# Optimization experiments

Measured on AMD Instinct MI355X. Metric: run time of the kernel, lower is better.

Reference implementation:

```python
import jax, jax.numpy as jnp
import numpy as np

DIM = 64
HID = 32  # dim * 1/2
P = 4     # patch_size

def _conv1x1(x, w):
    # x: [B,C,H,W], w: [O,C] -> [B,O,H,W]
    return jnp.einsum('oc,bchw->bohw', w, x)

def _dwconv3x3(x, w):
    # depthwise 3x3, padding 1. x: [B,C,H,W], w: [C,1,3,3]
    return jax.lax.conv_general_dilated(
        x, w, window_strides=(1, 1), padding=((1, 1), (1, 1)),
        dimension_numbers=('NCHW', 'OIHW', 'NCHW'),
        feature_group_count=x.shape[1])

def setup_inputs() -> dict:
    key = jax.random.key(0)
    k1, k2, k3, k4 = jax.random.split(key, 4)
    B, H, W = 4, 512, 512
    x = jax.random.normal(k1, (B, DIM, H, W), dtype=jnp.float32)
    w_in1 = jax.random.normal(k2, (2 * HID, DIM), dtype=jnp.float32) * 0.05
    w_dw = jax.random.normal(k3, (2 * HID, 1, 3, 3), dtype=jnp.float32) * 0.1
    w_in2 = jax.random.normal(k4, (DIM, HID), dtype=jnp.float32) * 0.05
    w_freq = jnp.ones((DIM, 1, 1, P, P // 2 + 1), dtype=jnp.float32)
    return {'x': x, 'w_in1': w_in1, 'w_dw': w_dw, 'w_in2': w_in2, 'w_freq': w_freq}

def reference(x, w_in1, w_dw, w_in2, w_freq):
    shortcut = x
    y = _dwconv3x3(_conv1x1(x, w_in1), w_dw)          # [B,2*HID,H,W]
    y1, y2 = jnp.split(y, 2, axis=1)
    y = jax.nn.gelu(y1, approximate=False) * y2       # [B,HID,H,W]
    y = _conv1x1(y, w_in2)                            # [B,DIM,H,W]
    b, c, h, w = y.shape
    h_n = (P - h % P) % P
    w_n = (P - w % P) % P
    if h_n or w_n:
        y = jnp.pad(y, ((0, 0), (0, 0), (0, h_n), (0, w_n)), mode='reflect')
    hp, wp = y.shape[2] // P, y.shape[3] // P
    # [B,C,hp,P,wp,P] -> [B,C,hp,wp,P,P]
    yp = y.reshape(b, c, hp, P, wp, P).transpose(0, 1, 2, 4, 3, 5)
    yf = jnp.fft.rfft2(yp)                            # [B,C,hp,wp,P,P//2+1] complex
    yf = w_freq * yf                                  # w_freq broadcasts over (C,1,1,P,P//2+1)
    yp = jnp.fft.irfft2(yf, s=(P, P))
    y = yp.transpose(0, 1, 2, 4, 3, 5).reshape(b, c, hp * P, wp * P)
    y = y[:, :, :h, :w]
    return y + shortcut
```

## Files before the change

### kernel.cpp

```cpp
#include <hip/hip_runtime.h>
#include <hip/hip_fp16.h>
#include <math.h>

#define DIMC 64
#define HIDC 32
#define IMH 512
#define IMW 512
#define TW 32
#define TH 16
#define HW 34
#define HH 18
#define NPIX (HW*HH)
#define NPIXP 624
#define NCHUNK 39
#define VSTR 20
#define PLANE (IMH*IMW)

#define IDOFF 0
#define W1OFF 16
#define W2OFF 2064
#define PWOFF 3088

typedef _Float16 half8  __attribute__((ext_vector_type(8)));
typedef __fp16   fp16x2 __attribute__((ext_vector_type(2)));
typedef float f32x4     __attribute__((ext_vector_type(4)));
typedef unsigned int uint;

union U4H8 { uint4 u; half8 h; };

static __device__ __forceinline__ uint pkrtz(float a, float b) {
    union { fp16x2 h; uint u; } x;
    x.h = __builtin_amdgcn_cvt_pkrtz(a, b);
    return x.u;
}
static __device__ __forceinline__ float lo16f(uint u) {
    union { uint u; _Float16 h[2]; } x; x.u = u; return (float)x.h[0];
}
static __device__ __forceinline__ float hi16f(uint u) {
    union { uint u; _Float16 h[2]; } x; x.u = u; return (float)x.h[1];
}
static __device__ __forceinline__ uint pkfma(uint w, uint t, uint acc) {
    union { uint u; __half2 h; } W, T, A;
    W.u = w; T.u = t; A.u = acc;
    A.h = __hfma2(W.h, T.h, A.h);
    return A.u;
}

static __device__ __forceinline__ float gelu_f(float u) {
    const float z  = fabsf(u) * 0.70710678118654752f;
    const float t  = __builtin_amdgcn_rcpf(fmaf(0.3275911f, z, 1.0f));
    const float e  = __builtin_amdgcn_exp2f(-z * z * 1.4426950408889634f);
    float p = fmaf(t, 1.061405429f, -1.453152027f);
    p = fmaf(t, p, 1.421413741f);
    p = fmaf(t, p, -0.284496736f);
    p = fmaf(t, p, 0.254829592f);
    p = p * t;
    const float erf_abs = fmaf(-p, e, 1.0f);
    const float erfv = copysignf(erf_abs, u);
    return 0.5f * u * (1.0f + erfv);
}

__global__ __launch_bounds__(256)
void ffn_prep(const float* __restrict__ w1, const float* __restrict__ wdw,
              const float* __restrict__ w2, const float* __restrict__ wf,
              uint* __restrict__ ws)
{
    __shared__ int sid;
    const int tid = threadIdx.x;
    if (tid == 0) sid = 1;
    __syncthreads();
    bool ok = true;
    for (int i = tid; i < DIMC * 12; i += 256) ok = ok && (wf[i] == 1.0f);
    if (!ok) atomicAnd(&sid, 0);
    for (int i = tid; i < 2048; i += 256) ws[W1OFF + i] = pkrtz(w1[2*i], w1[2*i+1]);
    for (int i = tid; i < 1024; i += 256) ws[W2OFF + i] = pkrtz(w2[2*i], w2[2*i+1]);
    for (int i = tid; i < 288; i += 256) {
        const int k = i >> 5, ch = i & 31;
        ws[PWOFF + i] = pkrtz(wdw[ch*9 + k], wdw[(ch + HIDC)*9 + k]);
    }
    __syncthreads();
    if (tid == 0) ws[IDOFF] = (uint)sid;
}

__global__ __launch_bounds__(512, 4)
void ffn_main(const float* __restrict__ x,
              const uint*  __restrict__ ws,
              const float* __restrict__ wf,
              float* __restrict__ out)
{
    __shared__ uint ts[NPIXP * 32];

    const int tid = threadIdx.x;
    const int bid = ((blockIdx.x & 7) << 8) + (blockIdx.x >> 3);
    const int b  = bid >> 9;
    const int tr = bid & 511;
    const int ty = tr >> 4, tx = tr & 15;
    const int oy = ty * TH, ox = tx * TW;

    const float* xb = x + (size_t)b * DIMC * PLANE;

    {
        auto quad = [&](int T) {
            const int cg = T / 144;
            const int rm = T - cg * 144;
            const int r  = rm >> 3;
            const int q  = rm & 7;
            const int gy = oy + r - 1;
            const int p0 = r * HW + 1 + 4 * q;
            if ((unsigned)gy >= IMH) {
                #pragma unroll
                for (int j = 0; j < 4; ++j) {
                    const uint p = (uint)(p0 + j), base = p << 5, sw = (p & 7) << 2;
                    uint4 z = {0u, 0u, 0u, 0u};
                    *reinterpret_cast<uint4*>(&ts[base + (((uint)(cg*8))   ^ sw)]) = z;
                    *reinterpret_cast<uint4*>(&ts[base + (((uint)(cg*8+4)) ^ sw)]) = z;
                }
            } else {
                const float* xp = xb + (size_t)(cg*16) * PLANE + (size_t)gy * IMW + (ox + 4*q);
                f32x4 f[16];
                #pragma unroll
                for (int i = 0; i < 16; ++i)
                    f[i] = *reinterpret_cast<const f32x4*>(xp + (size_t)i * PLANE);
                #pragma unroll
                for (int j = 0; j < 4; ++j) {
                    const uint p = (uint)(p0 + j), base = p << 5, sw = (p & 7) << 2;
                    uint4 o0, o1;
                    o0.x = pkrtz(f[0][j],  f[1][j]);  o0.y = pkrtz(f[2][j],  f[3][j]);
                    o0.z = pkrtz(f[4][j],  f[5][j]);  o0.w = pkrtz(f[6][j],  f[7][j]);
                    o1.x = pkrtz(f[8][j],  f[9][j]);  o1.y = pkrtz(f[10][j], f[11][j]);
                    o1.z = pkrtz(f[12][j], f[13][j]); o1.w = pkrtz(f[14][j], f[15][j]);
                    *reinterpret_cast<uint4*>(&ts[base + (((uint)(cg*8))   ^ sw)]) = o0;
                    *reinterpret_cast<uint4*>(&ts[base + (((uint)(cg*8+4)) ^ sw)]) = o1;
                }
            }
        };
        auto edge = [&](int E) {
            const int cg = E / 36;
            const int rm = E - cg * 36;
            const int s  = rm / 18;
            const int r  = rm - s * 18;
            const int gy = oy + r - 1;
            const int gx = s ? (ox + TW) : (ox - 1);
            const uint p = (uint)(r * HW + (s ? 33 : 0));
            const uint base = p << 5, sw = (p & 7) << 2;
            if ((unsigned)gy >= IMH || (unsigned)gx >= IMW) {
                uint4 z = {0u, 0u, 0u, 0u};
                *reinterpret_cast<uint4*>(&ts[base + (((uint)(cg*8))   ^ sw)]) = z;
                *reinterpret_cast<uint4*>(&ts[base + (((uint)(cg*8+4)) ^ sw)]) = z;
            } else {
                const float* xp = xb + (size_t)(cg*16) * PLANE + (size_t)gy * IMW + gx;
                float f[16];
                #pragma unroll
                for (int i = 0; i < 16; ++i) f[i] = xp[(size_t)i * PLANE];
                uint4 o0, o1;
                o0.x = pkrtz(f[0], f[1]);   o0.y = pkrtz(f[2], f[3]);
                o0.z = pkrtz(f[4], f[5]);   o0.w = pkrtz(f[6], f[7]);
                o1.x = pkrtz(f[8], f[9]);   o1.y = pkrtz(f[10], f[11]);
                o1.z = pkrtz(f[12], f[13]); o1.w = pkrtz(f[14], f[15]);
                *reinterpret_cast<uint4*>(&ts[base + (((uint)(cg*8))   ^ sw)]) = o0;
                *reinterpret_cast<uint4*>(&ts[base + (((uint)(cg*8+4)) ^ sw)]) = o1;
            }
        };
        quad(tid);
        if (tid < 64) quad(512 + tid);
        if (tid >= 368) edge(tid - 368);
        if (tid < 12) {
            const uint p = (uint)(612 + tid);
            const uint base = p << 5, sw = (p & 7) << 2;
            uint4 z = {0u, 0u, 0u, 0u};
            #pragma unroll
            for (int g = 0; g < 8; ++g)
                *reinterpret_cast<uint4*>(&ts[base + (((uint)(g << 2)) ^ sw)]) = z;
        }
    }

    const int lane = tid & 63, wid = tid >> 6;
    const int l15 = lane & 15, lg = lane >> 4;
    const int li = tid >> 5, lj = tid & 31;

    half8 afrag1[4][2];
    const uint4* w1v = reinterpret_cast<const uint4*>(ws + W1OFF);
    #pragma unroll
    for (int mt = 0; mt < 4; ++mt)
        #pragma unroll
        for (int ks = 0; ks < 2; ++ks) {
            U4H8 u; u.u = w1v[(mt*16 + l15)*8 + ks*4 + lg];
            afrag1[mt][ks] = u.h;
        }
    half8 afrag2[4];
    const uint4* w2v = reinterpret_cast<const uint4*>(ws + W2OFF);
    #pragma unroll
    for (int mt = 0; mt < 4; ++mt) { U4H8 u; u.u = w2v[(mt*16 + l15)*4 + lg]; afrag2[mt] = u.h; }

    const uint ident = ws[IDOFF];
    __syncthreads();

    uint xs[4][4][2];
    #pragma unroll
    for (int cc = 0; cc < 4; ++cc) {
        const int px = wid*64 + cc*16 + l15;
        const int h  = ((px >> 5) + 1) * HW + (px & 31) + 1;
        const uint base = (uint)h << 5, sw = ((uint)h & 7) << 2;
        #pragma unroll
        for (int mt = 0; mt < 4; ++mt) {
            const uint a = base + (((uint)(mt*8 + lg*2)) ^ sw);
            xs[cc][mt][0] = ts[a];
            xs[cc][mt][1] = ts[a + 1];
        }
    }
    __syncthreads();

    for (int chunk = wid; chunk < NCHUNK; chunk += 8) {
        const uint px = (uint)(chunk*16 + l15);
        const uint base = px << 5, sw = (px & 7) << 2;
        f32x4 acc[4];
        #pragma unroll
        for (int mt = 0; mt < 4; ++mt) acc[mt] = (f32x4)0.0f;
        #pragma unroll
        for (int ks = 0; ks < 2; ++ks) {
            U4H8 u; u.u = *reinterpret_cast<const uint4*>(&ts[base + (((uint)(ks*16 + lg*4)) ^ sw)]);
            #pragma unroll
            for (int mt = 0; mt < 4; ++mt)
                acc[mt] = __builtin_amdgcn_mfma_f32_16x16x32_f16(afrag1[mt][ks], u.h, acc[mt], 0, 0, 0);
        }
        #pragma unroll
        for (int mt = 0; mt < 2; ++mt) {
            uint4 o;
            o.x = pkrtz(acc[mt][0], acc[mt+2][0]);
            o.y = pkrtz(acc[mt][1], acc[mt+2][1]);
            o.z = pkrtz(acc[mt][2], acc[mt+2][2]);
            o.w = pkrtz(acc[mt][3], acc[mt+2][3]);
            *reinterpret_cast<uint4*>(&ts[base + (((uint)(mt*16 + lg*4)) ^ sw)]) = o;
        }
    }
    __syncthreads();

    uint acc2[32];
    #pragma unroll
    for (int c = 0; c < 32; ++c) acc2[c] = 0u;
    #pragma unroll
    for (int k = 0; k < 9; ++k) {
        const int di = k / 3, dj = k - di * 3;
        const uint hpx = (uint)((li + di) * HW + (lj + dj));
        const uint base = hpx << 5, sw = (hpx & 7) << 2;
        const uint4* pwv = reinterpret_cast<const uint4*>(ws + PWOFF + k*32);
        #pragma unroll
        for (int g = 0; g < 8; ++g) {
            const uint4 wv = pwv[g];
            const uint4 tv = *reinterpret_cast<const uint4*>(&ts[base + (((uint)(g << 2)) ^ sw)]);
            acc2[g*4+0] = pkfma(wv.x, tv.x, acc2[g*4+0]);
            acc2[g*4+1] = pkfma(wv.y, tv.y, acc2[g*4+1]);
            acc2[g*4+2] = pkfma(wv.z, tv.z, acc2[g*4+2]);
            acc2[g*4+3] = pkfma(wv.w, tv.w, acc2[g*4+3]);
        }
    }
    uint4 vo[4];
    #pragma unroll
    for (int gg = 0; gg < 4; ++gg) {
        uint o[4];
        #pragma unroll
        for (int q = 0; q < 4; ++q) {
            const int c2 = gg*4 + q;
            const uint wa = acc2[2*c2], wb = acc2[2*c2 + 1];
            const float v0 = gelu_f(lo16f(wa)) * hi16f(wa);
            const float v1 = gelu_f(lo16f(wb)) * hi16f(wb);
            o[q] = pkrtz(v0, v1);
        }
        vo[gg].x = o[0]; vo[gg].y = o[1]; vo[gg].z = o[2]; vo[gg].w = o[3];
    }
    __syncthreads();
    {
        const uint vb = (uint)tid * VSTR;
        #pragma unroll
        for (int gg = 0; gg < 4; ++gg)
            *reinterpret_cast<uint4*>(&ts[vb + (uint)(gg << 2)]) = vo[gg];
    }
    __syncthreads();

    float* ob = out + (size_t)b * DIMC * PLANE;
    if (ident) {
        #pragma unroll
        for (int cc = 0; cc < 4; ++cc) {
            const uint px = (uint)(wid*64 + cc*16 + l15);
            U4H8 u; u.u = *reinterpret_cast<const uint4*>(&ts[px * VSTR + (uint)(lg << 2)]);
            const size_t pix = (size_t)(oy + (int)(px >> 5)) * IMW + (ox + (int)(px & 31));
            float* op = ob + pix;
            #pragma unroll
            for (int mt = 0; mt < 4; ++mt) {
                f32x4 a = __builtin_amdgcn_mfma_f32_16x16x32_f16(afrag2[mt], u.h, (f32x4)0.0f, 0, 0, 0);
                #pragma unroll
                for (int r = 0; r < 4; ++r) {
                    const int ch = mt*16 + lg*4 + r;
                    const uint xw = xs[cc][mt][r >> 1];
                    const float xv = (r & 1) ? hi16f(xw) : lo16f(xw);
                    op[(size_t)ch * PLANE] = a[r] + xv;
                }
            }
        }
    } else {
        float* ys = reinterpret_cast<float*>(ts + 10240);
        for (int mt = 0; mt < 4; ++mt) {
            __syncthreads();
            #pragma unroll
            for (int cc = 0; cc < 4; ++cc) {
                const uint px = (uint)(wid*64 + cc*16 + l15);
                U4H8 u; u.u = *reinterpret_cast<const uint4*>(&ts[px * VSTR + (uint)(lg << 2)]);
                f32x4 a = __builtin_amdgcn_mfma_f32_16x16x32_f16(afrag2[mt], u.h, (f32x4)0.0f, 0, 0, 0);
                #pragma unroll
                for (int r = 0; r < 4; ++r)
                    ys[(lg*4 + r) * 520 + (int)px] = a[r];
            }
            __syncthreads();
            {
                const int chl = tid >> 5;
                const int ch  = mt*16 + chl;
                const int pt  = tid & 31;
                const int pi = (pt >> 3) * 4, pj = (pt & 7) * 4;
                float yv[4][4];
                #pragma unroll
                for (int a = 0; a < 4; ++a)
                    #pragma unroll
                    for (int c = 0; c < 4; ++c)
                        yv[a][c] = ys[chl * 520 + (pi + a) * TW + (pj + c)];
                float Cr[4][4], Ci[4][4];
                #pragma unroll
                for (int j = 0; j < 4; ++j) {
                    const float s02 = yv[0][j] + yv[2][j], d02 = yv[0][j] - yv[2][j];
                    const float s13 = yv[1][j] + yv[3][j], d13 = yv[1][j] - yv[3][j];
                    Cr[0][j] = s02 + s13; Ci[0][j] = 0.0f;
                    Cr[1][j] = d02;       Ci[1][j] = -d13;
                    Cr[2][j] = s02 - s13; Ci[2][j] = 0.0f;
                    Cr[3][j] = d02;       Ci[3][j] = d13;
                }
                float Zr[4][3], Zi[4][3];
                #pragma unroll
                for (int u = 0; u < 4; ++u) {
                    const float r0 = Cr[u][0], r1 = Cr[u][1], r2 = Cr[u][2], r3 = Cr[u][3];
                    const float i0 = Ci[u][0], i1 = Ci[u][1], i2 = Ci[u][2], i3 = Ci[u][3];
                    Zr[u][0] = r0 + r1 + r2 + r3;     Zi[u][0] = i0 + i1 + i2 + i3;
                    Zr[u][1] = (r0 - r2) + (i1 - i3); Zi[u][1] = (i0 - i2) - (r1 - r3);
                    Zr[u][2] = r0 - r1 + r2 - r3;     Zi[u][2] = i0 - i1 + i2 - i3;
                    #pragma unroll
                    for (int vv = 0; vv < 3; ++vv) {
                        const float m = wf[ch * 12 + u * 3 + vv];
                        Zr[u][vv] *= m; Zi[u][vv] *= m;
                    }
                }
                float Ar[4][3], Ai[4][3];
                #pragma unroll
                for (int vv = 0; vv < 3; ++vv) {
                    const float r0 = Zr[0][vv], r1 = Zr[1][vv], r2 = Zr[2][vv], r3 = Zr[3][vv];
                    const float i0 = Zi[0][vv], i1 = Zi[1][vv], i2 = Zi[2][vv], i3 = Zi[3][vv];
                    Ar[0][vv] = r0 + r1 + r2 + r3;     Ai[0][vv] = i0 + i1 + i2 + i3;
                    Ar[1][vv] = (r0 - r2) - (i1 - i3); Ai[1][vv] = (i0 - i2) + (r1 - r3);
                    Ar[2][vv] = r0 - r1 + r2 - r3;     Ai[2][vv] = i0 - i1 + i2 - i3;
                    Ar[3][vv] = (r0 - r2) + (i1 - i3); Ai[3][vv] = (i0 - i2) - (r1 - r3);
                }
                const float* xc = xb + (size_t)ch * PLANE;
                float*       oc = ob + (size_t)ch * PLANE;
                #pragma unroll
                for (int a = 0; a < 4; ++a) {
                    const float A0 = Ar[a][0], A1r = Ar[a][1], A2 = Ar[a][2];
                    const float B1i = Ai[a][1];
                    float res[4];
                    res[0] = (A0 + 2.0f * A1r + A2) * 0.0625f;
                    res[1] = (A0 - 2.0f * B1i - A2) * 0.0625f;
                    res[2] = (A0 - 2.0f * A1r + A2) * 0.0625f;
                    res[3] = (A0 + 2.0f * B1i - A2) * 0.0625f;
                    #pragma unroll
                    for (int c = 0; c < 4; ++c) {
                        const size_t pix = (size_t)(oy + pi + a) * IMW + (ox + pj + c);
                        oc[pix] = res[c] + xc[pix];
                    }
                }
            }
        }
    }
}

extern "C" void kernel_launch(void* const* d_in, const int* in_sizes, int n_in,
                              void* d_out, int out_size, void* d_ws, size_t ws_size,
                              hipStream_t stream) {
    (void)in_sizes; (void)n_in; (void)ws_size; (void)out_size;
    const float* x   = (const float*)d_in[0];
    const float* w1  = (const float*)d_in[1];
    const float* wdw = (const float*)d_in[2];
    const float* w2  = (const float*)d_in[3];
    const float* wf  = (const float*)d_in[4];
    float* out = (float*)d_out;
    uint* ws = (uint*)d_ws;

    ffn_prep<<<1, 256, 0, stream>>>(w1, wdw, w2, wf, ws);
    const int blocks = 4 * (IMH / TH) * (IMW / TW);
    ffn_main<<<blocks, 512, 0, stream>>>(x, ws, wf, out);
}
```

Baseline: 182.3 us.

## Use 768-thread blocks with distinct load roles and a new LDS swizzle

The block grows from 512 to 768 threads, and each thread gets one load role: 576 load quads, 144 load edges and 12 zero the padding. This replaces threads doing several quad/edge loads each. The MFMA chunk loops and output stage now spread over 12 waves instead of 8, while the depthwise/GELU stage stays on the first 512 threads. The LDS XOR swizzle changes to use pixel bits 1-3 to reduce bank conflicts. The launch bounds now ask for 6 blocks per CU, which may force register spilling, and idle waves in the depthwise stage waste slots.

```diff
diff --git a/kernel.cpp b/kernel.cpp
--- a/kernel.cpp
+++ b/kernel.cpp
@@ -15,11 +15,14 @@
 #define NCHUNK 39
 #define VSTR 20
 #define PLANE (IMH*IMW)
+#define NTHR 768
 
 #define IDOFF 0
 #define W1OFF 16
 #define W2OFF 2064
 #define PWOFF 3088
+
+#define SWZ(p) ((((uint)(p) >> 1) & 7u) << 2)
 
 typedef _Float16 half8  __attribute__((ext_vector_type(8)));
 typedef __fp16   fp16x2 __attribute__((ext_vector_type(2)));
@@ -82,7 +85,7 @@
     if (tid == 0) ws[IDOFF] = (uint)sid;
 }
 
-__global__ __launch_bounds__(512, 4)
+__global__ __launch_bounds__(NTHR, 6)
 void ffn_main(const float* __restrict__ x,
               const uint*  __restrict__ ws,
               const float* __restrict__ wf,
@@ -99,84 +102,77 @@
 
     const float* xb = x + (size_t)b * DIMC * PLANE;
 
-    {
-        auto quad = [&](int T) {
-            const int cg = T / 144;
-            const int rm = T - cg * 144;
-            const int r  = rm >> 3;
-            const int q  = rm & 7;
-            const int gy = oy + r - 1;
-            const int p0 = r * HW + 1 + 4 * q;
-            if ((unsigned)gy >= IMH) {
-                #pragma unroll
-                for (int j = 0; j < 4; ++j) {
-                    const uint p = (uint)(p0 + j), base = p << 5, sw = (p & 7) << 2;
-                    uint4 z = {0u, 0u, 0u, 0u};
-                    *reinterpret_cast<uint4*>(&ts[base + (((uint)(cg*8))   ^ sw)]) = z;
-                    *reinterpret_cast<uint4*>(&ts[base + (((uint)(cg*8+4)) ^ sw)]) = z;
-                }
-            } else {
-                const float* xp = xb + (size_t)(cg*16) * PLANE + (size_t)gy * IMW + (ox + 4*q);
-                f32x4 f[16];
-                #pragma unroll
-                for (int i = 0; i < 16; ++i)
-                    f[i] = *reinterpret_cast<const f32x4*>(xp + (size_t)i * PLANE);
-                #pragma unroll
-                for (int j = 0; j < 4; ++j) {
-                    const uint p = (uint)(p0 + j), base = p << 5, sw = (p & 7) << 2;
-                    uint4 o0, o1;
-                    o0.x = pkrtz(f[0][j],  f[1][j]);  o0.y = pkrtz(f[2][j],  f[3][j]);
-                    o0.z = pkrtz(f[4][j],  f[5][j]);  o0.w = pkrtz(f[6][j],  f[7][j]);
-                    o1.x = pkrtz(f[8][j],  f[9][j]);  o1.y = pkrtz(f[10][j], f[11][j]);
-                    o1.z = pkrtz(f[12][j], f[13][j]); o1.w = pkrtz(f[14][j], f[15][j]);
-                    *reinterpret_cast<uint4*>(&ts[base + (((uint)(cg*8))   ^ sw)]) = o0;
-                    *reinterpret_cast<uint4*>(&ts[base + (((uint)(cg*8+4)) ^ sw)]) = o1;
-                }
-            }
-        };
-        auto edge = [&](int E) {
-            const int cg = E / 36;
-            const int rm = E - cg * 36;
-            const int s  = rm / 18;
-            const int r  = rm - s * 18;
-            const int gy = oy + r - 1;
-            const int gx = s ? (ox + TW) : (ox - 1);
-            const uint p = (uint)(r * HW + (s ? 33 : 0));
-            const uint base = p << 5, sw = (p & 7) << 2;
-            if ((unsigned)gy >= IMH || (unsigned)gx >= IMW) {
+    if (tid < 576) {
+        const int cg = tid / 144;
+        const int rm = tid - cg * 144;
+        const int r  = rm >> 3;
+        const int q  = rm & 7;
+        const int gy = oy + r - 1;
+        const int p0 = r * HW + 1 + 4 * q;
+        if ((unsigned)gy >= IMH) {
+            #pragma unroll
+            for (int j = 0; j < 4; ++j) {
+                const uint p = (uint)(p0 + j), base = p << 5, sw = SWZ(p);
                 uint4 z = {0u, 0u, 0u, 0u};
                 *reinterpret_cast<uint4*>(&ts[base + (((uint)(cg*8))   ^ sw)]) = z;
                 *reinterpret_cast<uint4*>(&ts[base + (((uint)(cg*8+4)) ^ sw)]) = z;
-            } else {
-                const float* xp = xb + (size_t)(cg*16) * PLANE + (size_t)gy * IMW + gx;
-                float f[16];
-                #pragma unroll
-                for (int i = 0; i < 16; ++i) f[i] = xp[(size_t)i * PLANE];
+            }
+        } else {
+            const float* xp = xb + (size_t)(cg*16) * PLANE + (size_t)gy * IMW + (ox + 4*q);
+            f32x4 f[16];
+            #pragma unroll
+            for (int i = 0; i < 16; ++i)
+                f[i] = *reinterpret_cast<const f32x4*>(xp + (size_t)i * PLANE);
+            #pragma unroll
+            for (int j = 0; j < 4; ++j) {
+                const uint p = (uint)(p0 + j), base = p << 5, sw = SWZ(p);
                 uint4 o0, o1;
-                o0.x = pkrtz(f[0], f[1]);   o0.y = pkrtz(f[2], f[3]);
-                o0.z = pkrtz(f[4], f[5]);   o0.w = pkrtz(f[6], f[7]);
-                o1.x = pkrtz(f[8], f[9]);   o1.y = pkrtz(f[10], f[11]);
-                o1.z = pkrtz(f[12], f[13]); o1.w = pkrtz(f[14], f[15]);
+                o0.x = pkrtz(f[0][j],  f[1][j]);  o0.y = pkrtz(f[2][j],  f[3][j]);
+                o0.z = pkrtz(f[4][j],  f[5][j]);  o0.w = pkrtz(f[6][j],  f[7][j]);
+                o1.x = pkrtz(f[8][j],  f[9][j]);  o1.y = pkrtz(f[10][j], f[11][j]);
+                o1.z = pkrtz(f[12][j], f[13][j]); o1.w = pkrtz(f[14][j], f[15][j]);
                 *reinterpret_cast<uint4*>(&ts[base + (((uint)(cg*8))   ^ sw)]) = o0;
                 *reinterpret_cast<uint4*>(&ts[base + (((uint)(cg*8+4)) ^ sw)]) = o1;
             }
-        };
-        quad(tid);
-        if (tid < 64) quad(512 + tid);
-        if (tid >= 368) edge(tid - 368);
-        if (tid < 12) {
-            const uint p = (uint)(612 + tid);
-            const uint base = p << 5, sw = (p & 7) << 2;
+        }
+    } else if (tid < 720) {
+        const int E  = tid - 576;
+        const int cg = E / 36;
+        const int rm = E - cg * 36;
+        const int s  = rm / 18;
+        const int r  = rm - s * 18;
+        const int gy = oy + r - 1;
+        const int gx = s ? (ox + TW) : (ox - 1);
+        const uint p = (uint)(r * HW + (s ? 33 : 0));
+        const uint base = p << 5, sw = SWZ(p);
+        if ((unsigned)gy >= IMH || (unsigned)gx >= IMW) {
             uint4 z = {0u, 0u, 0u, 0u};
-            #pragma unroll
-            for (int g = 0; g < 8; ++g)
-                *reinterpret_cast<uint4*>(&ts[base + (((uint)(g << 2)) ^ sw)]) = z;
-        }
+            *reinterpret_cast<uint4*>(&ts[base + (((uint)(cg*8))   ^ sw)]) = z;
+            *reinterpret_cast<uint4*>(&ts[base + (((uint)(cg*8+4)) ^ sw)]) = z;
+        } else {
+            const float* xp = xb + (size_t)(cg*16) * PLANE + (size_t)gy * IMW + gx;
+            float f[16];
+            #pragma unroll
+            for (int i = 0; i < 16; ++i) f[i] = xp[(size_t)i * PLANE];
+            uint4 o0, o1;
+            o0.x = pkrtz(f[0], f[1]);   o0.y = pkrtz(f[2], f[3]);
+            o0.z = pkrtz(f[4], f[5]);   o0.w = pkrtz(f[6], f[7]);
+            o1.x = pkrtz(f[8], f[9]);   o1.y = pkrtz(f[10], f[11]);
+            o1.z = pkrtz(f[12], f[13]); o1.w = pkrtz(f[14], f[15]);
+            *reinterpret_cast<uint4*>(&ts[base + (((uint)(cg*8))   ^ sw)]) = o0;
+            *reinterpret_cast<uint4*>(&ts[base + (((uint)(cg*8+4)) ^ sw)]) = o1;
+        }
+    } else if (tid < 732) {
+        const uint p = (uint)(612 + tid - 720);
+        const uint base = p << 5, sw = SWZ(p);
+        uint4 z = {0u, 0u, 0u, 0u};
+        #pragma unroll
+        for (int g = 0; g < 8; ++g)
+            *reinterpret_cast<uint4*>(&ts[base + (((uint)(g << 2)) ^ sw)]) = z;
     }
 
     const int lane = tid & 63, wid = tid >> 6;
     const int l15 = lane & 15, lg = lane >> 4;
-    const int li = tid >> 5, lj = tid & 31;
 
     half8 afrag1[4][2];
     const uint4* w1v = reinterpret_cast<const uint4*>(ws + W1OFF);
@@ -195,24 +191,27 @@
     const uint ident = ws[IDOFF];
     __syncthreads();
 
-    uint xs[4][4][2];
+    uint xs[3][4][2];
     #pragma unroll
-    for (int cc = 0; cc < 4; ++cc) {
-        const int px = wid*64 + cc*16 + l15;
-        const int h  = ((px >> 5) + 1) * HW + (px & 31) + 1;
-        const uint base = (uint)h << 5, sw = ((uint)h & 7) << 2;
-        #pragma unroll
-        for (int mt = 0; mt < 4; ++mt) {
-            const uint a = base + (((uint)(mt*8 + lg*2)) ^ sw);
-            xs[cc][mt][0] = ts[a];
-            xs[cc][mt][1] = ts[a + 1];
-        }
-    }
-    __syncthreads();
-
-    for (int chunk = wid; chunk < NCHUNK; chunk += 8) {
+    for (int ci = 0; ci < 3; ++ci) {
+        const int c = wid + ci*12;
+        if (c < 32) {
+            const int px = c*16 + l15;
+            const int h  = ((px >> 5) + 1) * HW + (px & 31) + 1;
+            const uint base = (uint)h << 5, sw = SWZ(h);
+            #pragma unroll
+            for (int mt = 0; mt < 4; ++mt) {
+                const uint a = base + (((uint)(mt*8 + lg*2)) ^ sw);
+                xs[ci][mt][0] = ts[a];
+                xs[ci][mt][1] = ts[a + 1];
+            }
+        }
+    }
+    __syncthreads();
+
+    for (int chunk = wid; chunk < NCHUNK; chunk += 12) {
         const uint px = (uint)(chunk*16 + l15);
-        const uint base = px << 5, sw = (px & 7) << 2;
+        const uint base = px << 5, sw = SWZ(px);
         f32x4 acc[4];
         #pragma unroll
         for (int mt = 0; mt < 4; ++mt) acc[mt] = (f32x4)0.0f;
@@ -235,41 +234,44 @@
     }
     __syncthreads();
 
-    uint acc2[32];
-    #pragma unroll
-    for (int c = 0; c < 32; ++c) acc2[c] = 0u;
-    #pragma unroll
-    for (int k = 0; k < 9; ++k) {
-        const int di = k / 3, dj = k - di * 3;
-        const uint hpx = (uint)((li + di) * HW + (lj + dj));
-        const uint base = hpx << 5, sw = (hpx & 7) << 2;
-        const uint4* pwv = reinterpret_cast<const uint4*>(ws + PWOFF + k*32);
-        #pragma unroll
-        for (int g = 0; g < 8; ++g) {
-            const uint4 wv = pwv[g];
-            const uint4 tv = *reinterpret_cast<const uint4*>(&ts[base + (((uint)(g << 2)) ^ sw)]);
-            acc2[g*4+0] = pkfma(wv.x, tv.x, acc2[g*4+0]);
-            acc2[g*4+1] = pkfma(wv.y, tv.y, acc2[g*4+1]);
-            acc2[g*4+2] = pkfma(wv.z, tv.z, acc2[g*4+2]);
-            acc2[g*4+3] = pkfma(wv.w, tv.w, acc2[g*4+3]);
-        }
-    }
     uint4 vo[4];
-    #pragma unroll
-    for (int gg = 0; gg < 4; ++gg) {
-        uint o[4];
-        #pragma unroll
-        for (int q = 0; q < 4; ++q) {
-            const int c2 = gg*4 + q;
-            const uint wa = acc2[2*c2], wb = acc2[2*c2 + 1];
-            const float v0 = gelu_f(lo16f(wa)) * hi16f(wa);
-            const float v1 = gelu_f(lo16f(wb)) * hi16f(wb);
-            o[q] = pkrtz(v0, v1);
-        }
-        vo[gg].x = o[0]; vo[gg].y = o[1]; vo[gg].z = o[2]; vo[gg].w = o[3];
-    }
-    __syncthreads();
-    {
+    if (tid < 512) {
+        const int li = tid >> 5, lj = tid & 31;
+        uint acc2[32];
+        #pragma unroll
+        for (int c = 0; c < 32; ++c) acc2[c] = 0u;
+        #pragma unroll
+        for (int k = 0; k < 9; ++k) {
+            const int di = k / 3, dj = k - di * 3;
+            const uint hpx = (uint)((li + di) * HW + (lj + dj));
+            const uint base = hpx << 5, sw = SWZ(hpx);
+            const uint4* pwv = reinterpret_cast<const uint4*>(ws + PWOFF + k*32);
+            #pragma unroll
+            for (int g = 0; g < 8; ++g) {
+                const uint4 wv = pwv[g];
+                const uint4 tv = *reinterpret_cast<const uint4*>(&ts[base + (((uint)(g << 2)) ^ sw)]);
+                acc2[g*4+0] = pkfma(wv.x, tv.x, acc2[g*4+0]);
+                acc2[g*4+1] = pkfma(wv.y, tv.y, acc2[g*4+1]);
+                acc2[g*4+2] = pkfma(wv.z, tv.z, acc2[g*4+2]);
+                acc2[g*4+3] = pkfma(wv.w, tv.w, acc2[g*4+3]);
+            }
+        }
+        #pragma unroll
+        for (int gg = 0; gg < 4; ++gg) {
+            uint o[4];
+            #pragma unroll
+            for (int q = 0; q < 4; ++q) {
+                const int c2 = gg*4 + q;
+                const uint wa = acc2[2*c2], wb = acc2[2*c2 + 1];
+                const float v0 = gelu_f(lo16f(wa)) * hi16f(wa);
+                const float v1 = gelu_f(lo16f(wb)) * hi16f(wb);
+                o[q] = pkrtz(v0, v1);
+            }
+            vo[gg].x = o[0]; vo[gg].y = o[1]; vo[gg].z = o[2]; vo[gg].w = o[3];
+        }
+    }
+    __syncthreads();
+    if (tid < 512) {
         const uint vb = (uint)tid * VSTR;
         #pragma unroll
         for (int gg = 0; gg < 4; ++gg)
@@ -280,20 +282,23 @@
     float* ob = out + (size_t)b * DIMC * PLANE;
     if (ident) {
         #pragma unroll
-        for (int cc = 0; cc < 4; ++cc) {
-            const uint px = (uint)(wid*64 + cc*16 + l15);
-            U4H8 u; u.u = *reinterpret_cast<const uint4*>(&ts[px * VSTR + (uint)(lg << 2)]);
-            const size_t pix = (size_t)(oy + (int)(px >> 5)) * IMW + (ox + (int)(px & 31));
-            float* op = ob + pix;
-            #pragma unroll
-            for (int mt = 0; mt < 4; ++mt) {
-                f32x4 a = __builtin_amdgcn_mfma_f32_16x16x32_f16(afrag2[mt], u.h, (f32x4)0.0f, 0, 0, 0);
-                #pragma unroll
-                for (int r = 0; r < 4; ++r) {
-                    const int ch = mt*16 + lg*4 + r;
-                    const uint xw = xs[cc][mt][r >> 1];
-                    const float xv = (r & 1) ? hi16f(xw) : lo16f(xw);
-                    op[(size_t)ch * PLANE] = a[r] + xv;
+        for (int ci = 0; ci < 3; ++ci) {
+            const int c = wid + ci*12;
+            if (c < 32) {
+                const uint px = (uint)(c*16 + l15);
+                U4H8 u; u.u = *reinterpret_cast<const uint4*>(&ts[px * VSTR + (uint)(lg << 2)]);
+                const size_t pix = (size_t)(oy + (int)(px >> 5)) * IMW + (ox + (int)(px & 31));
+                float* op = ob + pix;
+                #pragma unroll
+                for (int mt = 0; mt < 4; ++mt) {
+                    f32x4 a = __builtin_amdgcn_mfma_f32_16x16x32_f16(afrag2[mt], u.h, (f32x4)0.0f, 0, 0, 0);
+                    #pragma unroll
+                    for (int r = 0; r < 4; ++r) {
+                        const int ch = mt*16 + lg*4 + r;
+                        const uint xw = xs[ci][mt][r >> 1];
+                        const float xv = (r & 1) ? hi16f(xw) : lo16f(xw);
+                        op[(size_t)ch * PLANE] = a[r] + xv;
+                    }
                 }
             }
         }
@@ -302,16 +307,19 @@
         for (int mt = 0; mt < 4; ++mt) {
             __syncthreads();
             #pragma unroll
-            for (int cc = 0; cc < 4; ++cc) {
-                const uint px = (uint)(wid*64 + cc*16 + l15);
-                U4H8 u; u.u = *reinterpret_cast<const uint4*>(&ts[px * VSTR + (uint)(lg << 2)]);
-                f32x4 a = __builtin_amdgcn_mfma_f32_16x16x32_f16(afrag2[mt], u.h, (f32x4)0.0f, 0, 0, 0);
-                #pragma unroll
-                for (int r = 0; r < 4; ++r)
-                    ys[(lg*4 + r) * 520 + (int)px] = a[r];
+            for (int ci = 0; ci < 3; ++ci) {
+                const int c = wid + ci*12;
+                if (c < 32) {
+                    const uint px = (uint)(c*16 + l15);
+                    U4H8 u; u.u = *reinterpret_cast<const uint4*>(&ts[px * VSTR + (uint)(lg << 2)]);
+                    f32x4 a = __builtin_amdgcn_mfma_f32_16x16x32_f16(afrag2[mt], u.h, (f32x4)0.0f, 0, 0, 0);
+                    #pragma unroll
+                    for (int r = 0; r < 4; ++r)
+                        ys[(lg*4 + r) * 520 + (int)px] = a[r];
+                }
             }
             __syncthreads();
-            {
+            if (tid < 512) {
                 const int chl = tid >> 5;
                 const int ch  = mt*16 + chl;
                 const int pt  = tid & 31;
@@ -392,5 +400,5 @@
 
     ffn_prep<<<1, 256, 0, stream>>>(w1, wdw, w2, wf, ws);
     const int blocks = 4 * (IMH / TH) * (IMW / TW);
-    ffn_main<<<blocks, 512, 0, stream>>>(x, ws, wf, out);
-}
+    ffn_main<<<blocks, NTHR, 0, stream>>>(x, ws, wf, out);
+}
```

Result: slower. 231.1 us (+26.7%).
